# Kernel tuning notes

Hardware: AMD Instinct MI355X
Metric: run time of the kernel (lower is better)

Reference implementation:

```python
import jax, jax.numpy as jnp
import numpy as np

B, HH, WW, DV, DC = 4, 128, 128, 768, 128
INNER = 2 * DV          # inner_ratio * values_dim = 1536
NH = 8                  # num_heads
DH = INNER // NH        # 192
SPACING = 4
COORDS_WEIGHT = 1.0     # attention_coords_weight
EPS = 1e-6


def _anchor_idx(h, w, s, shifted=False):
    rows = np.arange(0, h, s)
    cols = np.arange(0, w, s)
    if not shifted:
        rows = rows + ((h - 1) % s) // 2
        cols = cols + ((w - 1) % s) // 2
    return rows, cols


def _rms(x, w):
    return x * jax.lax.rsqrt(jnp.mean(x * x, axis=-1, keepdims=True) + EPS) * w


def _heads(x):  # (b, n, h*d) -> (b, h, n, d)
    b, n, _ = x.shape
    return x.reshape(b, n, NH, DH).transpose(0, 2, 1, 3)


def setup_inputs() -> dict:
    key = jax.random.key(0)
    ks = jax.random.split(key, 12)
    inp = {
        "values0": jax.random.normal(ks[0], (B, HH, WW, DV), jnp.float32),
        "coords0": jax.random.normal(ks[1], (B, HH, WW, DC), jnp.float32),
        "values1": jax.random.normal(ks[2], (B, HH, WW, DV), jnp.float32),
        "coords1": jax.random.normal(ks[3], (B, HH, WW, DC), jnp.float32),
        # values_to_qkv: Linear(DV, 3*INNER, bias=False), stored as (in, out)
        "w_qkv": jax.random.normal(ks[4], (DV, 3 * INNER), jnp.float32) * (DV ** -0.5),
        "qnorm_w": jnp.ones((INNER,), jnp.float32),
        "knorm_w": jnp.ones((INNER,), jnp.float32),
        # coords_to_qk: Linear(DC, 2*INNER, bias=False) + RMSNorm(2*INNER)
        "w_coords": jax.random.normal(ks[5], (DC, 2 * INNER), jnp.float32) * (DC ** -0.5),
        "coords_norm_w": jnp.ones((2 * INNER,), jnp.float32),
        "rel_pos_weight": jax.random.normal(ks[6], (1,), jnp.float32),
        # output_proj: Linear(INNER, DV)
        "out_w": jax.random.normal(ks[7], (INNER, DV), jnp.float32) * (INNER ** -0.5),
        "out_b": jnp.zeros((DV,), jnp.float32),
    }
    return inp


def reference(values0, coords0, values1, coords1, w_qkv, qnorm_w, knorm_w,
              w_coords, coords_norm_w, rel_pos_weight, out_w, out_b):
    rows, cols = _anchor_idx(HH, WW, SPACING)
    na = len(rows) * len(cols)  # anchors per source (1024)

    def gather(x):  # (B, HH, WW, D) -> (B, na, D)
        return x[:, rows[:, None], cols].reshape(B, na, -1)

    av = jnp.concatenate([gather(values0), gather(values1)], axis=1)  # (B, 2na, DV)
    ac = jnp.concatenate([gather(coords0), gather(coords1)], axis=1)  # (B, 2na, DC)

    qv, kv, vv = jnp.split(av @ w_qkv, 3, axis=-1)
    qv = _rms(qv, qnorm_w)
    kv = _rms(kv, knorm_w)
    qc, kc = jnp.split(_rms(ac @ w_coords, coords_norm_w), 2, axis=-1)

    qv, kv, vv, qc, kc = map(_heads, (qv, kv, vv, qc, kc))  # (B, NH, N, DH)

    scale = DH ** -0.5
    dots = jnp.einsum('bhqd,bhkd->bhqk', qv, kv) * scale
    rel = jnp.einsum('bhqd,bhkd->bhqk', qc, kc) * scale
    dots = dots + (rel_pos_weight[0] * COORDS_WEIGHT) * rel
    attn = jax.nn.softmax(dots, axis=-1)

    out = jnp.einsum('bhqk,bhkd->bhqd', attn, vv)          # (B, NH, N, DH)
    out = out.transpose(0, 2, 1, 3).reshape(B, 2 * na, INNER)
    out = out @ out_w + out_b                               # (B, 2na, DV)

    a0 = out[:, :na].reshape(B, len(rows), len(cols), DV)
    a1 = out[:, na:].reshape(B, len(rows), len(cols), DV)

    o0 = values0.at[:, rows[:, None], cols, :].add(a0)
    o1 = values1.at[:, rows[:, None], cols, :].add(a1)
    return jnp.stack([o0, o1])  # (2, B, HH, WW, DV)
```

## Files before the change

### kernel.cpp

```cpp
#include <hip/hip_runtime.h>

typedef unsigned short u16;
typedef unsigned int u32;
typedef float f32x4 __attribute__((ext_vector_type(4)));
typedef short bfx8 __attribute__((ext_vector_type(8)));
typedef u16 u16x8 __attribute__((ext_vector_type(8)));
typedef u16 u16x4 __attribute__((ext_vector_type(4)));

#define MFMA_BF16(a,b,c) __builtin_amdgcn_mfma_f32_16x16x32_bf16((a),(b),(c),0,0,0)
#define GL16(src, dst) __builtin_amdgcn_global_load_lds( \
    (const __attribute__((address_space(1))) u32*)(src), \
    (__attribute__((address_space(3))) u32*)(dst), 16, 0, 0)

__device__ __forceinline__ u16 f2bf(float f) {
  unsigned u = __float_as_uint(f);
  u += 0x7fffu + ((u >> 16) & 1u);
  return (u16)(u >> 16);
}
__device__ __forceinline__ float bf2f(u16 h) {
  return __uint_as_float((unsigned)h << 16);
}

#define SCALE_ATTN 0.07216878364870323f

__global__ __launch_bounds__(256) void wtrans_kernel(
    const float* __restrict__ in, u16* __restrict__ out, int K, int N)
{
  __shared__ float tile[32][33];
  int n0 = blockIdx.x * 32, k0 = blockIdx.y * 32;
  int tx = threadIdx.x, ty = threadIdx.y;
#pragma unroll
  for (int j = 0; j < 32; j += 8)
    tile[ty + j][tx] = in[(size_t)(k0 + ty + j) * N + n0 + tx];
  __syncthreads();
#pragma unroll
  for (int j = 0; j < 32; j += 8)
    out[(size_t)(n0 + ty + j) * K + k0 + tx] = f2bf(tile[tx][ty + j]);
}

__global__ __launch_bounds__(256) void gather_kernel(
    const float* __restrict__ v0, const float* __restrict__ c0,
    const float* __restrict__ v1, const float* __restrict__ c1,
    u16* __restrict__ av, u16* __restrict__ ac)
{
  int t = blockIdx.x;
  int b = t >> 11, n = t & 2047, s = n >> 10, a = n & 1023, rr = a >> 5, cc = a & 31;
  size_t pix = ((size_t)b * 128 + (1 + 4 * rr)) * 128 + (1 + 4 * cc);
  const float4* vs = (const float4*)((s ? v1 : v0) + pix * 768);
  const float4* cs = (const float4*)((s ? c1 : c0) + pix * 128);
  int tid = threadIdx.x;
  if (tid < 192) {
    float4 f = vs[tid];
    u16x4 o = { f2bf(f.x), f2bf(f.y), f2bf(f.z), f2bf(f.w) };
    *(u16x4*)(av + (size_t)t * 768 + tid * 4) = o;
  }
  if (tid < 32) {
    float4 f = cs[tid];
    u16x4 o = { f2bf(f.x), f2bf(f.y), f2bf(f.z), f2bf(f.w) };
    *(u16x4*)(ac + (size_t)t * 128 + tid * 4) = o;
  }
}

template<int EPILOG>
__global__ __launch_bounds__(256) void gemm128(
    const u16* __restrict__ A, const u16* __restrict__ Bt,
    int K, int lda, int ldb,
    u16* __restrict__ qp, u16* __restrict__ kp, u16* __restrict__ vT,
    float* __restrict__ outAdd, const float* __restrict__ bias)
{
  __shared__ u16 As[128 * 32];
  __shared__ u16 Bs[128 * 32];
  const int tid = threadIdx.x;
  const int wid = tid >> 6, lane = tid & 63;
  const int g = lane >> 4, q15 = lane & 15;
  const int wm = wid >> 1, wn = wid & 1;
  const int m0 = blockIdx.y * 128, n0 = blockIdx.x * 128;

  const u16* ga = A + (size_t)(m0 + (tid >> 2)) * lda + (tid & 3) * 8;
  const u16* gb = Bt + (size_t)(n0 + (tid >> 2)) * ldb + (tid & 3) * 8;
  u16* lA0 = &As[tid * 8]; u16* lA1 = &As[2048 + tid * 8];
  u16* lB0 = &Bs[tid * 8]; u16* lB1 = &Bs[2048 + tid * 8];
  const size_t a64 = (size_t)64 * lda, b64 = (size_t)64 * ldb;

  const f32x4 zero = {0.f, 0.f, 0.f, 0.f};
  f32x4 acc[4][4];
#pragma unroll
  for (int i = 0; i < 4; i++)
#pragma unroll
    for (int j = 0; j < 4; j++) acc[i][j] = zero;

  for (int kk = 0; kk < K; kk += 32) {
    GL16(ga + kk, lA0);
    GL16(ga + kk + a64, lA1);
    GL16(gb + kk, lB0);
    GL16(gb + kk + b64, lB1);
    __syncthreads();
    bfx8 af[4], bf[4];
#pragma unroll
    for (int mt = 0; mt < 4; mt++)
      af[mt] = *(const bfx8*)&As[(wm * 64 + mt * 16 + q15) * 32 + g * 8];
#pragma unroll
    for (int nt = 0; nt < 4; nt++)
      bf[nt] = *(const bfx8*)&Bs[(wn * 64 + nt * 16 + q15) * 32 + g * 8];
#pragma unroll
    for (int mt = 0; mt < 4; mt++)
#pragma unroll
      for (int nt = 0; nt < 4; nt++)
        acc[mt][nt] = MFMA_BF16(af[mt], bf[nt], acc[mt][nt]);
    __syncthreads();
  }

#pragma unroll
  for (int mt = 0; mt < 4; mt++) {
#pragma unroll
    for (int nt = 0; nt < 4; nt++) {
      const int tt = m0 + wm * 64 + mt * 16 + g * 4;
      const int c = n0 + wn * 64 + nt * 16 + q15;
      f32x4 v = acc[mt][nt];
      if (EPILOG == 0) {
        int isK = c >= 1536;
        int ck = isK ? c - 1536 : c;
        int hh = ck / 192, dd = ck - hh * 192;
#pragma unroll
        for (int j = 0; j < 4; j++) {
          int t = tt + j, b = t >> 11, n = t & 2047;
          size_t ro = ((size_t)(b * 8 + hh) * 2048 + n) * 384;
          u16 val = f2bf(v[j]);
          if (!isK) qp[ro + 192 + dd] = val;
          else      kp[ro + (size_t)((((24 + (dd >> 3)) ^ (n & 7)) << 3) + (dd & 7))] = val;
        }
      } else if (EPILOG == 1) {
        float bb = bias[c];
#pragma unroll
        for (int j = 0; j < 4; j++) {
          int t = tt + j, b = t >> 11, n = t & 2047;
          int s = n >> 10, a = n & 1023, rr = a >> 5, cc2 = a & 31;
          size_t orow = (size_t)(s * 4 + b) * 16384 + (size_t)(1 + 4 * rr) * 128 + (1 + 4 * cc2);
          outAdd[orow * 768 + c] += v[j] + bb;
        }
      } else {
        if (c < 1536) {
          int hh = c / 192, dd = c - hh * 192;
#pragma unroll
          for (int j = 0; j < 4; j++) {
            int t = tt + j, b = t >> 11, n = t & 2047;
            size_t ro = ((size_t)(b * 8 + hh) * 2048 + n) * 384;
            qp[ro + dd] = f2bf(v[j]);
          }
        } else if (c < 3072) {
          int ck = c - 1536;
          int hh = ck / 192, dd = ck - hh * 192;
          int chunk = dd >> 3, e = dd & 7;
#pragma unroll
          for (int j = 0; j < 4; j++) {
            int t = tt + j, b = t >> 11, n = t & 2047;
            size_t ro = ((size_t)(b * 8 + hh) * 2048 + n) * 384;
            kp[ro + (size_t)(((chunk ^ (n & 7)) << 3) + e)] = f2bf(v[j]);
          }
        } else {
          int cv = c - 3072;
          int hh = cv / 192, dv = cv - hh * 192;
          int t0 = tt, b = t0 >> 11, n = t0 & 2047;
          u16x4 o = { f2bf(v[0]), f2bf(v[1]), f2bf(v[2]), f2bf(v[3]) };
          *(u16x4*)(vT + ((size_t)(b * 8 + hh) * 192 + dv) * 2048 + n) = o;
        }
      }
    }
  }
}

__global__ __launch_bounds__(256) void rms_all_kernel(
    u16* __restrict__ qpack, u16* __restrict__ kpack,
    const float* __restrict__ qnw, const float* __restrict__ knw,
    const float* __restrict__ cnw, const float* __restrict__ relw)
{
  __shared__ float red[3][4];
  int t = blockIdx.x, tid = threadIdx.x;
  int b = t >> 11, n = t & 2047;
  float sqv = 0.f, skv = 0.f, sc = 0.f;
  u16x8 uqv, ukv, uqc, ukc;
  size_t ro = 0;
  int c = 0;
  if (tid < 192) {
    int h = tid / 24; c = tid % 24;
    ro = ((size_t)(b * 8 + h) * 2048 + n) * 384;
    uqv = *(const u16x8*)(qpack + ro + c * 8);
    ukv = *(const u16x8*)(kpack + ro + ((c ^ (n & 7)) * 8));
    uqc = *(const u16x8*)(qpack + ro + 192 + c * 8);
    ukc = *(const u16x8*)(kpack + ro + (((24 + c) ^ (n & 7)) * 8));
#pragma unroll
    for (int e = 0; e < 8; e++) {
      float a = bf2f(uqv[e]); sqv += a * a;
      float d = bf2f(ukv[e]); skv += d * d;
      float x = bf2f(uqc[e]); sc += x * x;
      float y = bf2f(ukc[e]); sc += y * y;
    }
  }
#pragma unroll
  for (int o = 32; o >= 1; o >>= 1) {
    sqv += __shfl_xor(sqv, o); skv += __shfl_xor(skv, o); sc += __shfl_xor(sc, o);
  }
  int wv = tid >> 6;
  if ((tid & 63) == 0) { red[0][wv] = sqv; red[1][wv] = skv; red[2][wv] = sc; }
  __syncthreads();
  sqv = red[0][0] + red[0][1] + red[0][2] + red[0][3];
  skv = red[1][0] + red[1][1] + red[1][2] + red[1][3];
  sc  = red[2][0] + red[2][1] + red[2][2] + red[2][3];
  float fqv = rsqrtf(sqv * (1.f / 1536.f) + 1e-6f) * SCALE_ATTN;
  float fkv = rsqrtf(skv * (1.f / 1536.f) + 1e-6f);
  float fc  = rsqrtf(sc * (1.f / 3072.f) + 1e-6f);
  float fqc = fc * SCALE_ATTN * relw[0];
  if (tid < 192) {
    u16x8 o0, o1, o2, o3;
#pragma unroll
    for (int e = 0; e < 8; e++) {
      int col = tid * 8 + e;
      o0[e] = f2bf(bf2f(uqv[e]) * fqv * qnw[col]);
      o1[e] = f2bf(bf2f(ukv[e]) * fkv * knw[col]);
      o2[e] = f2bf(bf2f(uqc[e]) * fqc * cnw[col]);
      o3[e] = f2bf(bf2f(ukc[e]) * fc  * cnw[1536 + col]);
    }
    *(u16x8*)(qpack + ro + c * 8) = o0;
    *(u16x8*)(kpack + ro + ((c ^ (n & 7)) * 8)) = o1;
    *(u16x8*)(qpack + ro + 192 + c * 8) = o2;
    *(u16x8*)(kpack + ro + (((24 + c) ^ (n & 7)) * 8)) = o3;
  }
}

__global__ __launch_bounds__(256, 2) void attn_kernel(
    const u16* __restrict__ qpack, const u16* __restrict__ kpack,
    const u16* __restrict__ vT, u16* __restrict__ attnO,
    const float* __restrict__ cpy_v0, const float* __restrict__ cpy_v1,
    float* __restrict__ cpy_out)
{
  __shared__ u16 Ks[2][32 * 384];
  __shared__ u16 Vs[2][192 * 32];

  const int tid = threadIdx.x;
  const int wid = tid >> 6, lane = tid & 63;
  const int g = lane >> 4, q15 = lane & 15;
  const int bid = blockIdx.x;
  const int bh = (bid & 7) * 4 + ((bid >> 3) >> 4);
  const int q0 = ((bid >> 3) & 15) * 128 + wid * 32;
  const int b = bh >> 3, h = bh & 7;
  const int sw = q15 & 7;
  const int vsw = g ^ (q15 & 3);
  const bool hi = g >= 2;
  const int srcA = q15 + ((g & 1) << 5);

  const f32x4* cs0 = (const f32x4*)cpy_v0;
  const f32x4* cs1 = (const f32x4*)cpy_v1;
  f32x4* cdst = (f32x4*)cpy_out;
  const size_t cgid = (size_t)bid * 256 + tid;
  const size_t CHALF = 12582912ull;
  const size_t CSLAB = 8388608ull;

  bfx8 qf[2][12];
  {
    const u16* qb = qpack + ((size_t)bh * 2048 + q0 + q15) * 384 + g * 8;
#pragma unroll
    for (int s = 0; s < 2; s++)
#pragma unroll
      for (int c = 0; c < 12; c++)
        qf[s][c] = *(const bfx8*)(qb + s * 16 * 384 + c * 32);
  }

  const f32x4 zero = {0.f, 0.f, 0.f, 0.f};
  f32x4 acc[2][12];
#pragma unroll
  for (int s = 0; s < 2; s++)
#pragma unroll
    for (int i = 0; i < 12; i++) acc[s][i] = zero;
  float m0 = -3e30f, m1 = -3e30f, l0 = 0.f, l1 = 0.f;

  const char* kg = (const char*)(kpack + (size_t)bh * 2048 * 384);
  const char* vg = (const char*)(vT + (size_t)bh * 192 * 2048);

  auto stage = [&](int buf, int kb) {
    const char* ks = kg + (size_t)kb * 768;
#pragma unroll
    for (int j = 0; j < 6; j++) {
      int off = j * 4096 + tid * 16;
      GL16(ks + off, (char*)&Ks[buf][0] + off);
    }
    const char* vsrc = vg + (size_t)kb * 2;
#pragma unroll
    for (int j = 0; j < 3; j++) {
      int off = j * 4096 + tid * 16;
      int row = off >> 6;
      int cc = (tid & 3) ^ (row & 3);
      GL16(vsrc + (size_t)row * 4096 + cc * 16, (char*)&Vs[buf][0] + off);
    }
  };

  stage(0, 0);
  asm volatile("s_waitcnt vmcnt(0)" ::: "memory");
  __builtin_amdgcn_s_barrier();

  int cur = 0;
  f32x4 cr0, cr1, cr2;
  for (int t = 0; t < 64; t++) {
    if (t > 0) {
      const size_t pb = (size_t)(t - 1) * 131072ull + cgid;
      __builtin_nontemporal_store(cr0, &cdst[pb]);
      __builtin_nontemporal_store(cr1, &cdst[pb + CSLAB]);
      __builtin_nontemporal_store(cr2, &cdst[pb + 2 * CSLAB]);
    }
    if (t < 63) stage(cur ^ 1, (t + 1) * 32);
    {
      const size_t i0 = (size_t)t * 131072ull + cgid;
      const size_t i1 = i0 + CSLAB, i2 = i0 + 2 * CSLAB;
      cr0 = __builtin_nontemporal_load(&cs0[i0]);
      cr1 = (i1 < CHALF) ? __builtin_nontemporal_load(&cs0[i1])
                         : __builtin_nontemporal_load(&cs1[i1 - CHALF]);
      cr2 = __builtin_nontemporal_load(&cs1[i2 - CHALF]);
    }

    f32x4 s00 = zero, s01 = zero, s10 = zero, s11 = zero;
    const u16* Kc = &Ks[cur][0];
    __builtin_amdgcn_s_setprio(1);
#pragma unroll
    for (int c = 0; c < 12; c++) {
      int ch = ((((c << 2) + g) ^ sw) << 3);
      bfx8 k0 = *(const bfx8*)(Kc + q15 * 384 + ch);
      bfx8 k1 = *(const bfx8*)(Kc + (q15 + 16) * 384 + ch);
      s00 = MFMA_BF16(k0, qf[0][c], s00);
      s01 = MFMA_BF16(k0, qf[1][c], s01);
      s10 = MFMA_BF16(k1, qf[0][c], s10);
      s11 = MFMA_BF16(k1, qf[1][c], s11);
    }
    __builtin_amdgcn_s_setprio(0);

    float bm0 = fmaxf(fmaxf(fmaxf(s00[0], s00[1]), fmaxf(s00[2], s00[3])),
                      fmaxf(fmaxf(s10[0], s10[1]), fmaxf(s10[2], s10[3])));
    float bm1 = fmaxf(fmaxf(fmaxf(s01[0], s01[1]), fmaxf(s01[2], s01[3])),
                      fmaxf(fmaxf(s11[0], s11[1]), fmaxf(s11[2], s11[3])));

    if (__any((bm0 > m0 + 8.f) | (bm1 > m1 + 8.f))) {
      bm0 = fmaxf(bm0, __shfl_xor(bm0, 16)); bm0 = fmaxf(bm0, __shfl_xor(bm0, 32));
      bm1 = fmaxf(bm1, __shfl_xor(bm1, 16)); bm1 = fmaxf(bm1, __shfl_xor(bm1, 32));
      float n0 = fmaxf(m0, bm0), n1 = fmaxf(m1, bm1);
      float c0 = __expf(m0 - n0), c1 = __expf(m1 - n1);
      l0 *= c0; l1 *= c1;
#pragma unroll
      for (int i = 0; i < 12; i++) {
#pragma unroll
        for (int j = 0; j < 4; j++) { acc[0][i][j] *= c0; acc[1][i][j] *= c1; }
      }
      m0 = n0; m1 = n1;
    }

    float p0[8], p1[8];
    float rs0 = 0.f, rs1 = 0.f;
#pragma unroll
    for (int j = 0; j < 4; j++) {
      p0[j]     = __expf(s00[j] - m0);
      p0[4 + j] = __expf(s10[j] - m0);
      p1[j]     = __expf(s01[j] - m1);
      p1[4 + j] = __expf(s11[j] - m1);
      rs0 += p0[j] + p0[4 + j];
      rs1 += p1[j] + p1[4 + j];
    }
    l0 += rs0; l1 += rs1;

    union { bfx8 v; u32 w[4]; } pt0, pt1;
    {
      u32 w0 = (u32)f2bf(p0[0]) | ((u32)f2bf(p0[1]) << 16);
      u32 w1 = (u32)f2bf(p0[2]) | ((u32)f2bf(p0[3]) << 16);
      u32 w2 = (u32)f2bf(p0[4]) | ((u32)f2bf(p0[5]) << 16);
      u32 w3 = (u32)f2bf(p0[6]) | ((u32)f2bf(p0[7]) << 16);
      u32 a0 = __shfl((int)w0, srcA),      b0 = __shfl((int)w2, srcA);
      u32 a1 = __shfl((int)w1, srcA),      b1 = __shfl((int)w3, srcA);
      u32 a2 = __shfl((int)w0, srcA + 16), b2 = __shfl((int)w2, srcA + 16);
      u32 a3 = __shfl((int)w1, srcA + 16), b3 = __shfl((int)w3, srcA + 16);
      pt0.w[0] = hi ? b0 : a0; pt0.w[1] = hi ? b1 : a1;
      pt0.w[2] = hi ? b2 : a2; pt0.w[3] = hi ? b3 : a3;
    }
    {
      u32 w0 = (u32)f2bf(p1[0]) | ((u32)f2bf(p1[1]) << 16);
      u32 w1 = (u32)f2bf(p1[2]) | ((u32)f2bf(p1[3]) << 16);
      u32 w2 = (u32)f2bf(p1[4]) | ((u32)f2bf(p1[5]) << 16);
      u32 w3 = (u32)f2bf(p1[6]) | ((u32)f2bf(p1[7]) << 16);
      u32 a0 = __shfl((int)w0, srcA),      b0 = __shfl((int)w2, srcA);
      u32 a1 = __shfl((int)w1, srcA),      b1 = __shfl((int)w3, srcA);
      u32 a2 = __shfl((int)w0, srcA + 16), b2 = __shfl((int)w2, srcA + 16);
      u32 a3 = __shfl((int)w1, srcA + 16), b3 = __shfl((int)w3, srcA + 16);
      pt1.w[0] = hi ? b0 : a0; pt1.w[1] = hi ? b1 : a1;
      pt1.w[2] = hi ? b2 : a2; pt1.w[3] = hi ? b3 : a3;
    }

    const u16* Vc = &Vs[cur][0];
    __builtin_amdgcn_s_setprio(1);
#pragma unroll
    for (int dt = 0; dt < 12; dt++) {
      bfx8 vf = *(const bfx8*)(Vc + dt * 512 + q15 * 32 + vsw * 8);
      acc[0][dt] = MFMA_BF16(vf, pt0.v, acc[0][dt]);
      acc[1][dt] = MFMA_BF16(vf, pt1.v, acc[1][dt]);
    }
    __builtin_amdgcn_s_setprio(0);

    asm volatile("s_waitcnt vmcnt(3)" ::: "memory");
    __builtin_amdgcn_s_barrier();
    cur ^= 1;
  }

  {
    const size_t pb = (size_t)63 * 131072ull + cgid;
    __builtin_nontemporal_store(cr0, &cdst[pb]);
    __builtin_nontemporal_store(cr1, &cdst[pb + CSLAB]);
    __builtin_nontemporal_store(cr2, &cdst[pb + 2 * CSLAB]);
  }

  l0 += __shfl_xor(l0, 16); l0 += __shfl_xor(l0, 32);
  l1 += __shfl_xor(l1, 16); l1 += __shfl_xor(l1, 32);

  float li0 = 1.f / l0, li1 = 1.f / l1;
  u16* ob = attnO + ((size_t)(b * 2048 + q0 + q15)) * 1536 + h * 192;
#pragma unroll
  for (int dt = 0; dt < 12; dt++) {
    u16x4 o0, o1;
#pragma unroll
    for (int j = 0; j < 4; j++) {
      o0[j] = f2bf(acc[0][dt][j] * li0);
      o1[j] = f2bf(acc[1][dt][j] * li1);
    }
    *(u16x4*)(ob + dt * 16 + g * 4) = o0;
    *(u16x4*)(ob + (size_t)16 * 1536 + dt * 16 + g * 4) = o1;
  }
}

extern "C" void kernel_launch(void* const* d_in, const int* in_sizes, int n_in,
                              void* d_out, int out_size, void* d_ws, size_t ws_size,
                              hipStream_t stream)
{
  const float* values0 = (const float*)d_in[0];
  const float* coords0 = (const float*)d_in[1];
  const float* values1 = (const float*)d_in[2];
  const float* coords1 = (const float*)d_in[3];
  const float* w_qkv   = (const float*)d_in[4];
  const float* qnorm_w = (const float*)d_in[5];
  const float* knorm_w = (const float*)d_in[6];
  const float* w_coords= (const float*)d_in[7];
  const float* cnorm_w = (const float*)d_in[8];
  const float* relw    = (const float*)d_in[9];
  const float* out_w   = (const float*)d_in[10];
  const float* out_b   = (const float*)d_in[11];
  float* out = (float*)d_out;
  (void)in_sizes; (void)n_in; (void)out_size; (void)ws_size;

  char* ws = (char*)d_ws;
  u16* qpack   = (u16*)(ws);
  u16* kpack   = (u16*)(ws + 50331648ull);
  u16* vT      = (u16*)(ws + 100663296ull);
  u16* attnO   = (u16*)(ws + 125829120ull);
  u16* av      = (u16*)(ws + 150994944ull);
  u16* ac      = (u16*)(ws + 163577856ull);
  u16* wqkvT   = (u16*)(ws + 165675008ull);
  u16* wcoordT = (u16*)(ws + 172752896ull);
  u16* outwT   = (u16*)(ws + 173539328ull);

  wtrans_kernel<<<dim3(144, 24), dim3(32, 8), 0, stream>>>(w_qkv, wqkvT, 768, 4608);
  wtrans_kernel<<<dim3(96, 4),   dim3(32, 8), 0, stream>>>(w_coords, wcoordT, 128, 3072);
  wtrans_kernel<<<dim3(24, 48),  dim3(32, 8), 0, stream>>>(out_w, outwT, 1536, 768);
  gather_kernel<<<8192, 256, 0, stream>>>(values0, coords0, values1, coords1, av, ac);

  gemm128<2><<<dim3(36, 64), 256, 0, stream>>>(av, wqkvT, 768, 768, 768,
                                               qpack, kpack, vT, nullptr, nullptr);
  gemm128<0><<<dim3(24, 64), 256, 0, stream>>>(ac, wcoordT, 128, 128, 128,
                                               qpack, kpack, nullptr, nullptr, nullptr);

  rms_all_kernel<<<8192, 256, 0, stream>>>(qpack, kpack, qnorm_w, knorm_w, cnorm_w, relw);

  attn_kernel<<<512, 256, 0, stream>>>(qpack, kpack, vT, attnO,
                                       values0, values1, out);

  gemm128<1><<<dim3(6, 64), 256, 0, stream>>>(attnO, outwT, 1536, 1536, 1536,
                                              nullptr, nullptr, nullptr, out, out_b);
}
```

Before: 489.6 us.

## Use 8 waves per attention block with 16 query rows per wave

The attention kernel now launches 512 threads per block, and each wave handles 16 query rows instead of 32. This halves the per-wave Q fragments, accumulators and softmax state, so more waves can be resident, and the K/V tile staging is spread over more threads. The fused copy of values into the output is reorganised into 48 iterations of two slabs each, with wait counts adjusted to match. The cost is that every wave re-reads the full K/V tiles from LDS for half as much MFMA work, which lowers compute per LDS read.

```diff
diff --git a/kernel.cpp b/kernel.cpp
--- a/kernel.cpp
+++ b/kernel.cpp
@@ -227,7 +227,7 @@
   }
 }
 
-__global__ __launch_bounds__(256, 2) void attn_kernel(
+__global__ __launch_bounds__(512, 4) void attn_kernel(
     const u16* __restrict__ qpack, const u16* __restrict__ kpack,
     const u16* __restrict__ vT, u16* __restrict__ attnO,
     const float* __restrict__ cpy_v0, const float* __restrict__ cpy_v1,
@@ -241,7 +241,7 @@
   const int g = lane >> 4, q15 = lane & 15;
   const int bid = blockIdx.x;
   const int bh = (bid & 7) * 4 + ((bid >> 3) >> 4);
-  const int q0 = ((bid >> 3) & 15) * 128 + wid * 32;
+  const int q0 = ((bid >> 3) & 15) * 128 + wid * 16;
   const int b = bh >> 3, h = bh & 7;
   const int sw = q15 & 7;
   const int vsw = g ^ (q15 & 3);
@@ -251,27 +251,23 @@
   const f32x4* cs0 = (const f32x4*)cpy_v0;
   const f32x4* cs1 = (const f32x4*)cpy_v1;
   f32x4* cdst = (f32x4*)cpy_out;
-  const size_t cgid = (size_t)bid * 256 + tid;
+  const size_t cgid = (size_t)bid * 512 + tid;
   const size_t CHALF = 12582912ull;
-  const size_t CSLAB = 8388608ull;
-
-  bfx8 qf[2][12];
+  const size_t CSLAB = 262144ull;
+
+  bfx8 qf[12];
   {
     const u16* qb = qpack + ((size_t)bh * 2048 + q0 + q15) * 384 + g * 8;
 #pragma unroll
-    for (int s = 0; s < 2; s++)
-#pragma unroll
-      for (int c = 0; c < 12; c++)
-        qf[s][c] = *(const bfx8*)(qb + s * 16 * 384 + c * 32);
+    for (int c = 0; c < 12; c++)
+      qf[c] = *(const bfx8*)(qb + c * 32);
   }
 
   const f32x4 zero = {0.f, 0.f, 0.f, 0.f};
-  f32x4 acc[2][12];
-#pragma unroll
-  for (int s = 0; s < 2; s++)
-#pragma unroll
-    for (int i = 0; i < 12; i++) acc[s][i] = zero;
-  float m0 = -3e30f, m1 = -3e30f, l0 = 0.f, l1 = 0.f;
+  f32x4 acc[12];
+#pragma unroll
+  for (int i = 0; i < 12; i++) acc[i] = zero;
+  float m0 = -3e30f, l0 = 0.f;
 
   const char* kg = (const char*)(kpack + (size_t)bh * 2048 * 384);
   const char* vg = (const char*)(vT + (size_t)bh * 192 * 2048);
@@ -279,17 +275,19 @@
   auto stage = [&](int buf, int kb) {
     const char* ks = kg + (size_t)kb * 768;
 #pragma unroll
-    for (int j = 0; j < 6; j++) {
-      int off = j * 4096 + tid * 16;
+    for (int j = 0; j < 3; j++) {
+      int off = j * 8192 + tid * 16;
       GL16(ks + off, (char*)&Ks[buf][0] + off);
     }
-    const char* vsrc = vg + (size_t)kb * 2;
-#pragma unroll
-    for (int j = 0; j < 3; j++) {
-      int off = j * 4096 + tid * 16;
-      int row = off >> 6;
-      int cc = (tid & 3) ^ (row & 3);
-      GL16(vsrc + (size_t)row * 4096 + cc * 16, (char*)&Vs[buf][0] + off);
+    if (tid < 384) {
+      const char* vsrc = vg + (size_t)kb * 2;
+#pragma unroll
+      for (int j = 0; j < 2; j++) {
+        int off = j * 6144 + tid * 16;
+        int row = off >> 6;
+        int cc = (tid & 3) ^ (row & 3);
+        GL16(vsrc + (size_t)row * 4096 + cc * 16, (char*)&Vs[buf][0] + off);
+      }
     }
   };
 
@@ -298,25 +296,22 @@
   __builtin_amdgcn_s_barrier();
 
   int cur = 0;
-  f32x4 cr0, cr1, cr2;
+  f32x4 cr0, cr1;
   for (int t = 0; t < 64; t++) {
-    if (t > 0) {
-      const size_t pb = (size_t)(t - 1) * 131072ull + cgid;
-      __builtin_nontemporal_store(cr0, &cdst[pb]);
-      __builtin_nontemporal_store(cr1, &cdst[pb + CSLAB]);
-      __builtin_nontemporal_store(cr2, &cdst[pb + 2 * CSLAB]);
+    if (t >= 1 && t <= 48) {
+      const size_t pd = (size_t)(2 * (t - 1)) * CSLAB + cgid;
+      __builtin_nontemporal_store(cr0, &cdst[pd]);
+      __builtin_nontemporal_store(cr1, &cdst[pd + CSLAB]);
     }
     if (t < 63) stage(cur ^ 1, (t + 1) * 32);
-    {
-      const size_t i0 = (size_t)t * 131072ull + cgid;
-      const size_t i1 = i0 + CSLAB, i2 = i0 + 2 * CSLAB;
-      cr0 = __builtin_nontemporal_load(&cs0[i0]);
-      cr1 = (i1 < CHALF) ? __builtin_nontemporal_load(&cs0[i1])
-                         : __builtin_nontemporal_load(&cs1[i1 - CHALF]);
-      cr2 = __builtin_nontemporal_load(&cs1[i2 - CHALF]);
-    }
-
-    f32x4 s00 = zero, s01 = zero, s10 = zero, s11 = zero;
+    if (t < 48) {
+      const size_t s0 = (size_t)(2 * t) * CSLAB + cgid;
+      cr0 = __builtin_nontemporal_load(t < 24 ? &cs0[s0] : &cs1[s0 - CHALF]);
+      cr1 = __builtin_nontemporal_load(t < 24 ? &cs0[s0 + CSLAB]
+                                              : &cs1[s0 + CSLAB - CHALF]);
+    }
+
+    f32x4 s00 = zero, s10 = zero;
     const u16* Kc = &Ks[cur][0];
     __builtin_amdgcn_s_setprio(1);
 #pragma unroll
@@ -324,46 +319,38 @@
       int ch = ((((c << 2) + g) ^ sw) << 3);
       bfx8 k0 = *(const bfx8*)(Kc + q15 * 384 + ch);
       bfx8 k1 = *(const bfx8*)(Kc + (q15 + 16) * 384 + ch);
-      s00 = MFMA_BF16(k0, qf[0][c], s00);
-      s01 = MFMA_BF16(k0, qf[1][c], s01);
-      s10 = MFMA_BF16(k1, qf[0][c], s10);
-      s11 = MFMA_BF16(k1, qf[1][c], s11);
+      s00 = MFMA_BF16(k0, qf[c], s00);
+      s10 = MFMA_BF16(k1, qf[c], s10);
     }
     __builtin_amdgcn_s_setprio(0);
 
     float bm0 = fmaxf(fmaxf(fmaxf(s00[0], s00[1]), fmaxf(s00[2], s00[3])),
                       fmaxf(fmaxf(s10[0], s10[1]), fmaxf(s10[2], s10[3])));
-    float bm1 = fmaxf(fmaxf(fmaxf(s01[0], s01[1]), fmaxf(s01[2], s01[3])),
-                      fmaxf(fmaxf(s11[0], s11[1]), fmaxf(s11[2], s11[3])));
-
-    if (__any((bm0 > m0 + 8.f) | (bm1 > m1 + 8.f))) {
+
+    if (__any(bm0 > m0 + 8.f)) {
       bm0 = fmaxf(bm0, __shfl_xor(bm0, 16)); bm0 = fmaxf(bm0, __shfl_xor(bm0, 32));
-      bm1 = fmaxf(bm1, __shfl_xor(bm1, 16)); bm1 = fmaxf(bm1, __shfl_xor(bm1, 32));
-      float n0 = fmaxf(m0, bm0), n1 = fmaxf(m1, bm1);
-      float c0 = __expf(m0 - n0), c1 = __expf(m1 - n1);
-      l0 *= c0; l1 *= c1;
+      float n0 = fmaxf(m0, bm0);
+      float c0 = __expf(m0 - n0);
+      l0 *= c0;
 #pragma unroll
       for (int i = 0; i < 12; i++) {
 #pragma unroll
-        for (int j = 0; j < 4; j++) { acc[0][i][j] *= c0; acc[1][i][j] *= c1; }
+        for (int j = 0; j < 4; j++) acc[i][j] *= c0;
       }
-      m0 = n0; m1 = n1;
-    }
-
-    float p0[8], p1[8];
-    float rs0 = 0.f, rs1 = 0.f;
+      m0 = n0;
+    }
+
+    float p0[8];
+    float rs0 = 0.f;
 #pragma unroll
     for (int j = 0; j < 4; j++) {
       p0[j]     = __expf(s00[j] - m0);
       p0[4 + j] = __expf(s10[j] - m0);
-      p1[j]     = __expf(s01[j] - m1);
-      p1[4 + j] = __expf(s11[j] - m1);
       rs0 += p0[j] + p0[4 + j];
-      rs1 += p1[j] + p1[4 + j];
-    }
-    l0 += rs0; l1 += rs1;
-
-    union { bfx8 v; u32 w[4]; } pt0, pt1;
+    }
+    l0 += rs0;
+
+    union { bfx8 v; u32 w[4]; } pt0;
     {
       u32 w0 = (u32)f2bf(p0[0]) | ((u32)f2bf(p0[1]) << 16);
       u32 w1 = (u32)f2bf(p0[2]) | ((u32)f2bf(p0[3]) << 16);
@@ -376,56 +363,33 @@
       pt0.w[0] = hi ? b0 : a0; pt0.w[1] = hi ? b1 : a1;
       pt0.w[2] = hi ? b2 : a2; pt0.w[3] = hi ? b3 : a3;
     }
-    {
-      u32 w0 = (u32)f2bf(p1[0]) | ((u32)f2bf(p1[1]) << 16);
-      u32 w1 = (u32)f2bf(p1[2]) | ((u32)f2bf(p1[3]) << 16);
-      u32 w2 = (u32)f2bf(p1[4]) | ((u32)f2bf(p1[5]) << 16);
-      u32 w3 = (u32)f2bf(p1[6]) | ((u32)f2bf(p1[7]) << 16);
-      u32 a0 = __shfl((int)w0, srcA),      b0 = __shfl((int)w2, srcA);
-      u32 a1 = __shfl((int)w1, srcA),      b1 = __shfl((int)w3, srcA);
-      u32 a2 = __shfl((int)w0, srcA + 16), b2 = __shfl((int)w2, srcA + 16);
-      u32 a3 = __shfl((int)w1, srcA + 16), b3 = __shfl((int)w3, srcA + 16);
-      pt1.w[0] = hi ? b0 : a0; pt1.w[1] = hi ? b1 : a1;
-      pt1.w[2] = hi ? b2 : a2; pt1.w[3] = hi ? b3 : a3;
-    }
 
     const u16* Vc = &Vs[cur][0];
     __builtin_amdgcn_s_setprio(1);
 #pragma unroll
     for (int dt = 0; dt < 12; dt++) {
       bfx8 vf = *(const bfx8*)(Vc + dt * 512 + q15 * 32 + vsw * 8);
-      acc[0][dt] = MFMA_BF16(vf, pt0.v, acc[0][dt]);
-      acc[1][dt] = MFMA_BF16(vf, pt1.v, acc[1][dt]);
+      acc[dt] = MFMA_BF16(vf, pt0.v, acc[dt]);
     }
     __builtin_amdgcn_s_setprio(0);
 
-    asm volatile("s_waitcnt vmcnt(3)" ::: "memory");
+    if (t < 48) asm volatile("s_waitcnt vmcnt(2)" ::: "memory");
+    else        asm volatile("s_waitcnt vmcnt(0)" ::: "memory");
     __builtin_amdgcn_s_barrier();
     cur ^= 1;
   }
 
-  {
-    const size_t pb = (size_t)63 * 131072ull + cgid;
-    __builtin_nontemporal_store(cr0, &cdst[pb]);
-    __builtin_nontemporal_store(cr1, &cdst[pb + CSLAB]);
-    __builtin_nontemporal_store(cr2, &cdst[pb + 2 * CSLAB]);
-  }
-
   l0 += __shfl_xor(l0, 16); l0 += __shfl_xor(l0, 32);
-  l1 += __shfl_xor(l1, 16); l1 += __shfl_xor(l1, 32);
-
-  float li0 = 1.f / l0, li1 = 1.f / l1;
+
+  float li0 = 1.f / l0;
   u16* ob = attnO + ((size_t)(b * 2048 + q0 + q15)) * 1536 + h * 192;
 #pragma unroll
   for (int dt = 0; dt < 12; dt++) {
-    u16x4 o0, o1;
-#pragma unroll
-    for (int j = 0; j < 4; j++) {
-      o0[j] = f2bf(acc[0][dt][j] * li0);
-      o1[j] = f2bf(acc[1][dt][j] * li1);
-    }
+    u16x4 o0;
+#pragma unroll
+    for (int j = 0; j < 4; j++)
+      o0[j] = f2bf(acc[dt][j] * li0);
     *(u16x4*)(ob + dt * 16 + g * 4) = o0;
-    *(u16x4*)(ob + (size_t)16 * 1536 + dt * 16 + g * 4) = o1;
   }
 }
 
@@ -471,7 +435,7 @@
 
   rms_all_kernel<<<8192, 256, 0, stream>>>(qpack, kpack, qnorm_w, knorm_w, cnorm_w, relw);
 
-  attn_kernel<<<512, 256, 0, stream>>>(qpack, kpack, vT, attnO,
+  attn_kernel<<<512, 512, 0, stream>>>(qpack, kpack, vT, attnO,
                                        values0, values1, out);
 
   gemm128<1><<<dim3(6, 64), 256, 0, stream>>>(attnO, outwT, 1536, 1536, 1536,
```

Measured after the change: 643.4 us. 31.4% more time.
